# Kernel tuning notes

Hardware: AMD Instinct MI355X
Metric: run time of the kernel (lower is better)

## Reference

```python
import jax, jax.numpy as jnp
import numpy as np

C = 128
N_ATOMS = 3584          # 512 * 7 bands
DILATIONS = (1, 3, 9, 27, 81, 1)
NEG = 0.2               # leaky_relu slope used throughout the repo
B, T = 8, 2048


def lrelu(x):
    return jnp.where(x >= 0, x, NEG * x)


def setup_inputs() -> dict:
    key = jax.random.key(0)
    keys = iter(jax.random.split(key, 40))

    def rn(shape, scale=0.05):
        return jax.random.normal(next(keys), shape, jnp.float32) * scale

    # x: [B, 4, T]; channel 0 = atom index (stored as float, cast with .long() in forward),
    # channels 1:3 = (pos, amp), channel 3 = band size (unused by forward)
    atoms = jax.random.randint(next(keys), (B, 1, T), 0, N_ATOMS).astype(jnp.float32)
    pos_amp = jax.random.normal(next(keys), (B, 2, T), jnp.float32)
    band = jnp.zeros((B, 1, T), jnp.float32)
    x = jnp.concatenate([atoms, pos_amp, band], axis=1)

    nl = len(DILATIONS)
    return {
        "x": x,
        "embed_w": rn((N_ATOMS, C), 0.1),
        "posamp_w": rn((C, 2), 0.1), "posamp_b": jnp.zeros((C,), jnp.float32),
        "reduce_w": rn((C, 2 * C)), "reduce_b": jnp.zeros((C,), jnp.float32),
        "dil_w": rn((nl, C, C, 3)), "dil_b": jnp.zeros((nl, C), jnp.float32),
        "one_w": rn((nl, C, C)), "one_b": jnp.zeros((nl, C), jnp.float32),
        "atom_w1": rn((C, C)), "atom_b1": jnp.zeros((C,), jnp.float32),
        "atom_w2": rn((C, C)), "atom_b2": jnp.zeros((C,), jnp.float32),
        "atom_w3": rn((N_ATOMS, C)), "atom_b3": jnp.zeros((N_ATOMS,), jnp.float32),
        "pa_w1": rn((C, C)), "pa_b1": jnp.zeros((C,), jnp.float32),
        "pa_w2": rn((C, C)), "pa_b2": jnp.zeros((C,), jnp.float32),
        "pa_w3": rn((2, C)), "pa_b3": jnp.zeros((2,), jnp.float32),
    }


def _linear_stack(h, w1, b1, w2, b2, w3, b3):
    # LinearOutputStack(channels, 3, out_channels=...): two hidden linears with
    # leaky_relu, final linear with no activation.
    h = lrelu(h @ w1.T + b1)
    h = lrelu(h @ w2.T + b2)
    return h @ w3.T + b3


def reference(x, embed_w, posamp_w, posamp_b, reduce_w, reduce_b,
              dil_w, dil_b, one_w, one_b,
              atom_w1, atom_b1, atom_w2, atom_b2, atom_w3, atom_b3,
              pa_w1, pa_b1, pa_w2, pa_b2, pa_w3, pa_b3):
    xt = jnp.transpose(x, (0, 2, 1))                              # [B,T,4]
    idx = jax.lax.stop_gradient(xt[:, :, 0]).astype(jnp.int32)    # atom ids
    at = embed_w[idx]                                             # [B,T,C] gather
    pa = xt[:, :, 1:3] @ posamp_w.T + posamp_b                    # [B,T,C]
    h = jnp.concatenate([at, pa], axis=-1)                        # [B,T,2C]
    h = h @ reduce_w.T + reduce_b                                 # 1x1 conv == linear
    h = jnp.transpose(h, (0, 2, 1))                               # [B,C,T]

    # DilatedStack: residual blocks (dilated k=3 conv -> 1x1 conv -> +res -> lrelu)
    for i, d in enumerate(DILATIONS):
        orig = h
        y = jax.lax.conv_general_dilated(
            h, dil_w[i], window_strides=(1,), padding=[(d, d)],
            rhs_dilation=(d,), dimension_numbers=('NCH', 'OIH', 'NCH'))
        y = y + dil_b[i][None, :, None]
        y = jnp.einsum('oc,bct->bot', one_w[i], y) + one_b[i][None, :, None]
        h = lrelu(y + orig)

    ht = jnp.transpose(h, (0, 2, 1))                              # [B,T,C]
    # Original applies the output stacks over all T, then slices the last step.
    a = _linear_stack(ht, atom_w1, atom_b1, atom_w2, atom_b2, atom_w3, atom_b3)[:, -1:, :]
    pa_out = _linear_stack(ht, pa_w1, pa_b1, pa_w2, pa_b2, pa_w3, pa_b3)[:, -1:, :]
    return a, pa_out
```

## Files before the change

kernel.cpp:

```cpp
#include <hip/hip_runtime.h>

#define CCH 128
#define TLEN 2048
#define NBATCH 8
#define NATOMS 3584
#define NEG 0.2f
typedef unsigned long long ull;

#define PK1(a) ((ull)(a))
#define PK2(a,b) (PK1(a)|((ull)(b)<<7))
#define PK3(a,b,c) (PK2(a,b)|((ull)(c)<<14))
#define PK4(a,b,c,d) (PK3(a,b,c)|((ull)(d)<<21))
#define PK5(a,b,c,d,e) (PK4(a,b,c,d)|((ull)(e)<<28))

__device__ const int g_l2cols[28] = {
    9,10,18,19,27,28,36,37,45,46,54,55,63,64,
    72,73,81,82,90,91,99,100,108,109,117,118,126,127};

__device__ __forceinline__ float lrelu(float v) { return v >= 0.f ? v : NEG * v; }
__device__ __forceinline__ float dot4(float4 w, float4 x) {
    return w.x * x.x + w.y * x.y + w.z * x.z + w.w * x.w;
}

__device__ __forceinline__ float red16x4(float a0, float a1, float a2, float a3, int s) {
    a0 += __shfl_xor(a0, 8); a1 += __shfl_xor(a1, 8);
    a2 += __shfl_xor(a2, 8); a3 += __shfl_xor(a3, 8);
    a0 += __shfl_xor(a0, 4); a1 += __shfl_xor(a1, 4);
    a2 += __shfl_xor(a2, 4); a3 += __shfl_xor(a3, 4);
    float u0 = (s & 2) ? a2 : a0;
    float v0 = (s & 2) ? a0 : a2;
    u0 += __shfl_xor(v0, 2);
    float u1 = (s & 2) ? a3 : a1;
    float v1 = (s & 2) ? a1 : a3;
    u1 += __shfl_xor(v1, 2);
    float w  = (s & 1) ? u1 : u0;
    float vv = (s & 1) ? u0 : u1;
    w += __shfl_xor(vv, 1);
    return w;
}

template<int NB>
__device__ __forceinline__ void conv4(
        const float (*src)[CCH], float (*dst)[CCH], float* gout,
        ull pm, ull pc, ull pp, ull pd, int a0,
        const float* __restrict__ Wd, const float* __restrict__ bd,
        const float* __restrict__ Wo, const float* __restrict__ bo,
        float (*ybuf)[CCH], int g, int s)
{
    const int ch = 4 * g + (s & 3);
    const float myBd = bd[ch];
    const float myBo = bo[ch];
    float4 W[24], V[8];
    {
        const float4* Wr = (const float4*)Wd + (size_t)(4 * g) * 96;
        #pragma unroll
        for (int r = 0; r < 4; ++r)
            #pragma unroll
            for (int j = 0; j < 3; ++j) {
                W[r * 6 + j]     = Wr[r * 96 + 3 * s + j];
                W[r * 6 + 3 + j] = Wr[r * 96 + 3 * s + 48 + j];
            }
        const float4* Or = (const float4*)Wo + (size_t)(4 * g) * 32;
        #pragma unroll
        for (int r = 0; r < 4; ++r) {
            V[r * 2]     = Or[r * 32 + s];
            V[r * 2 + 1] = Or[r * 32 + s + 16];
        }
    }
    __syncthreads();
    #pragma unroll
    for (int t = 0; t < NB; ++t) {
        const float* fm = src[(int)((pm >> (7 * t)) & 127)];
        const float* fc = src[(int)((pc >> (7 * t)) & 127)];
        const float* fp = src[(int)((pp >> (7 * t)) & 127)];
        float4 m0 = *(const float4*)(fm + 4 * s);
        float4 m1 = *(const float4*)(fm + 4 * s + 64);
        float4 c0 = *(const float4*)(fc + 4 * s);
        float4 c1 = *(const float4*)(fc + 4 * s + 64);
        float4 p0 = *(const float4*)(fp + 4 * s);
        float4 p1 = *(const float4*)(fp + 4 * s + 64);
        float acc[4];
        #pragma unroll
        for (int r = 0; r < 4; ++r) {
            float4 wA = W[r*6+0], wB = W[r*6+1], wC = W[r*6+2];
            float a = wA.x*m0.x + wA.y*c0.x + wA.z*p0.x + wA.w*m0.y
                    + wB.x*c0.y + wB.y*p0.y + wB.z*m0.z + wB.w*c0.z
                    + wC.x*p0.z + wC.y*m0.w + wC.z*c0.w + wC.w*p0.w;
            float4 wD = W[r*6+3], wE = W[r*6+4], wF = W[r*6+5];
            float b2 = wD.x*m1.x + wD.y*c1.x + wD.z*p1.x + wD.w*m1.y
                     + wE.x*c1.y + wE.y*p1.y + wE.z*m1.z + wE.w*c1.z
                     + wF.x*p1.z + wF.y*m1.w + wF.z*c1.w + wF.w*p1.w;
            acc[r] = a + b2;
        }
        float tot = red16x4(acc[0], acc[1], acc[2], acc[3], s);
        if (s < 4) ybuf[t][ch] = tot + myBd;
    }
    __syncthreads();
    #pragma unroll
    for (int t = 0; t < NB; ++t) {
        int jc = (int)((pc >> (7 * t)) & 127);
        int jd = (int)((pd >> (7 * t)) & 127);
        const float* y = ybuf[t];
        float4 y0 = *(const float4*)(y + 4 * s);
        float4 y1 = *(const float4*)(y + 4 * s + 64);
        float a0_ = dot4(V[0], y0) + dot4(V[1], y1);
        float a1_ = dot4(V[2], y0) + dot4(V[3], y1);
        float a2_ = dot4(V[4], y0) + dot4(V[5], y1);
        float a3_ = dot4(V[6], y0) + dot4(V[7], y1);
        float tot = red16x4(a0_, a1_, a2_, a3_, s);
        if (s < 4) {
            float h = lrelu(tot + myBo + src[jc][ch]);
            if (gout) gout[ch] = h;
            else      dst[jd][ch] = (a0 + jd < 128) ? h : 0.f;
        }
    }
}

__device__ __forceinline__ void mlp4(
        const float* hin, float* hout,
        const float* __restrict__ w, const float* __restrict__ bv,
        int g, int s)
{
    const int ch = 4 * g + (s & 3);
    const float myB = bv[ch];
    float4 V[8];
    const float4* r = (const float4*)w + (size_t)(4 * g) * 32;
    #pragma unroll
    for (int rr = 0; rr < 4; ++rr) {
        V[rr * 2]     = r[rr * 32 + s];
        V[rr * 2 + 1] = r[rr * 32 + s + 16];
    }
    __syncthreads();
    float4 x0 = *(const float4*)(hin + 4 * s);
    float4 x1 = *(const float4*)(hin + 4 * s + 64);
    float a0_ = dot4(V[0], x0) + dot4(V[1], x1);
    float a1_ = dot4(V[2], x0) + dot4(V[3], x1);
    float a2_ = dot4(V[4], x0) + dot4(V[5], x1);
    float a3_ = dot4(V[6], x0) + dot4(V[7], x1);
    float tot = red16x4(a0_, a1_, a2_, a3_, s);
    if (s < 4) hout[ch] = lrelu(tot + myB);
}

__global__ void __launch_bounds__(512, 2) k_cone(
        const float* __restrict__ x,
        const float* __restrict__ embed_w,
        const float* __restrict__ posamp_w,
        const float* __restrict__ posamp_b,
        const float* __restrict__ reduce_w,
        const float* __restrict__ reduce_b,
        const float* __restrict__ dil_w,
        const float* __restrict__ dil_b,
        const float* __restrict__ one_w,
        const float* __restrict__ one_b,
        float* __restrict__ l2c)
{
    const int i   = blockIdx.x;
    const int b   = blockIdx.y;
    const int own = g_l2cols[i];
    const int a0  = own - 4;
    const int tid = threadIdx.x;
    const int g   = tid >> 4;
    const int s   = tid & 15;
    const int ch  = 4 * g + (s & 3);

    __shared__ float A[9][CCH];
    __shared__ float B[8][CCH];
    __shared__ float cat[9][2 * CCH];
    __shared__ float ybuf[3][CCH];

    const float* xb = x + b * 4 * TLEN;
    for (int v = tid; v < 9 * 256; v += 512) {
        int p   = v >> 8;
        int chv = v & 255;
        int ab  = a0 + p;
        float val = 0.f;
        if (ab < 128) {
            int t = (TLEN - 128) + ab;
            if (chv < CCH) {
                int idx = (int)xb[t];
                val = embed_w[idx * CCH + chv];
            } else {
                int cc = chv - CCH;
                val = posamp_w[2 * cc] * xb[TLEN + t]
                    + posamp_w[2 * cc + 1] * xb[2 * TLEN + t] + posamp_b[cc];
            }
        }
        cat[p][chv] = val;
    }
    float4 RW[16];
    const float4* rw = (const float4*)reduce_w + (size_t)(4 * g) * 64;
    #pragma unroll
    for (int r = 0; r < 4; ++r)
        #pragma unroll
        for (int j = 0; j < 4; ++j)
            RW[r * 4 + j] = rw[r * 64 + s + 16 * j];
    const float rb = reduce_b[ch];
    __syncthreads();

    #pragma unroll 3
    for (int t = 0; t < 9; ++t) {
        const float* sc = cat[t];
        float4 x0 = *(const float4*)(sc + 4 * s);
        float4 x1 = *(const float4*)(sc + 4 * s + 64);
        float4 x2 = *(const float4*)(sc + 4 * s + 128);
        float4 x3 = *(const float4*)(sc + 4 * s + 192);
        float a0_ = dot4(RW[0], x0) + dot4(RW[1], x1) + dot4(RW[2], x2) + dot4(RW[3], x3);
        float a1_ = dot4(RW[4], x0) + dot4(RW[5], x1) + dot4(RW[6], x2) + dot4(RW[7], x3);
        float a2_ = dot4(RW[8], x0) + dot4(RW[9], x1) + dot4(RW[10], x2) + dot4(RW[11], x3);
        float a3_ = dot4(RW[12], x0) + dot4(RW[13], x1) + dot4(RW[14], x2) + dot4(RW[15], x3);
        float tot = red16x4(a0_, a1_, a2_, a3_, s);
        if (s < 4) A[t][ch] = (a0 + t < 128) ? tot + rb : 0.f;
    }

    conv4<3>(A, B, nullptr,
             PK3(0,3,6), PK3(1,4,7), PK3(2,5,8), PK3(1,4,7), a0,
             dil_w, dil_b, one_w, one_b, ybuf, g, s);
    conv4<1>(B, B, l2c + (size_t)(b * 28 + i) * CCH,
             PK1(1), PK1(4), PK1(7), PK1(4), a0,
             dil_w + (size_t)1 * CCH * CCH * 3, dil_b + CCH,
             one_w + (size_t)1 * CCH * CCH, one_b + CCH, ybuf, g, s);
}

__global__ void __launch_bounds__(512, 2) k_tail(
        const float* __restrict__ l2c,
        const float* __restrict__ dil_w,
        const float* __restrict__ dil_b,
        const float* __restrict__ one_w,
        const float* __restrict__ one_b,
        const float* __restrict__ aw1, const float* __restrict__ ab1,
        const float* __restrict__ aw2, const float* __restrict__ ab2,
        const float* __restrict__ pw1, const float* __restrict__ pb1,
        const float* __restrict__ pw2, const float* __restrict__ pb2,
        const float* __restrict__ pw3, const float* __restrict__ pb3,
        float* __restrict__ h2w,
        float* __restrict__ out)
{
    const int b   = blockIdx.x;
    const int tid = threadIdx.x;
    const int g   = tid >> 4;
    const int s   = tid & 15;

    __shared__ float E[29][CCH];
    __shared__ float D[11][CCH];
    __shared__ float B2[5][CCH];
    __shared__ float C2[3][CCH];
    __shared__ float HF[CCH];
    __shared__ float ybuf[5][CCH];
    __shared__ float h1a[CCH], h1p[CCH], h2p[CCH];

    if (tid < CCH) { E[28][tid] = 0.f; D[10][tid] = 0.f; B2[4][tid] = 0.f; C2[2][tid] = 0.f; }
    for (int v = tid; v < 28 * 32; v += 512) {
        int col = v >> 5, f4i = v & 31;
        *(float4*)&E[col][f4i * 4] =
            *(const float4*)(l2c + (size_t)(b * 28 + col) * CCH + f4i * 4);
    }

    const float* Wd3 = dil_w + (size_t)2 * CCH * CCH * 3;
    const float* bd3 = dil_b + 2 * CCH;
    const float* Wo3 = one_w + (size_t)2 * CCH * CCH;
    const float* bo3 = one_b + 2 * CCH;
    conv4<5>(E, D, nullptr,
             PK5(0,1,6,7,12), PK5(2,3,8,9,14), PK5(4,5,10,11,16),
             PK5(0,1,2,3,4), -1000, Wd3, bd3, Wo3, bo3, ybuf, g, s);
    conv4<5>(E, D, nullptr,
             PK5(13,18,19,24,25), PK5(15,20,21,26,27), PK5(17,22,23,28,28),
             PK5(5,6,7,8,9), -1000, Wd3, bd3, Wo3, bo3, ybuf, g, s);

    conv4<4>(D, B2, nullptr,
             PK4(0,1,6,7), PK4(2,3,8,9), PK4(4,5,10,10), PK4(0,1,2,3), -1000,
             dil_w + (size_t)3 * CCH * CCH * 3, dil_b + 3 * CCH,
             one_w + (size_t)3 * CCH * CCH, one_b + 3 * CCH, ybuf, g, s);
    conv4<2>(B2, C2, nullptr,
             PK2(0,1), PK2(2,3), PK2(4,4), PK2(0,1), -1000,
             dil_w + (size_t)4 * CCH * CCH * 3, dil_b + 4 * CCH,
             one_w + (size_t)4 * CCH * CCH, one_b + 4 * CCH, ybuf, g, s);
    conv4<1>(C2, C2, HF,
             PK1(0), PK1(1), PK1(2), PK1(0), -1000,
             dil_w + (size_t)5 * CCH * CCH * 3, dil_b + 5 * CCH,
             one_w + (size_t)5 * CCH * CCH, one_b + 5 * CCH, ybuf, g, s);

    mlp4(HF, h1a, aw1, ab1, g, s);
    mlp4(HF, h1p, pw1, pb1, g, s);
    mlp4(h1a, h2w + b * CCH, aw2, ab2, g, s);
    mlp4(h1p, h2p, pw2, pb2, g, s);
    __syncthreads();

    if (tid < 64) {
        int row = tid >> 5, q = tid & 31;
        float4 w4 = *(const float4*)(pw3 + row * CCH + 4 * q);
        float4 xv = *(const float4*)(h2p + 4 * q);
        float acc = dot4(w4, xv);
        acc += __shfl_xor(acc, 1);
        acc += __shfl_xor(acc, 2);
        acc += __shfl_xor(acc, 4);
        acc += __shfl_xor(acc, 8);
        acc += __shfl_xor(acc, 16);
        if (q == 0) out[NBATCH * NATOMS + b * 2 + row] = acc + pb3[row];
    }
}

__global__ void __launch_bounds__(512) k_head(
        const float* __restrict__ h2w,
        const float* __restrict__ aw3, const float* __restrict__ ab3,
        float* __restrict__ out)
{
    const int b   = blockIdx.y;
    const int row = blockIdx.x * 512 + threadIdx.x;
    __shared__ float hs[CCH];
    if (threadIdx.x < 32)
        *(float4*)&hs[threadIdx.x * 4] =
            *(const float4*)(h2w + b * CCH + threadIdx.x * 4);
    __syncthreads();

    const float4* r = (const float4*)(aw3 + (size_t)row * CCH);
    float s0 = 0.f, s1 = 0.f, s2 = 0.f, s3 = 0.f;
    #pragma unroll
    for (int k = 0; k < 32; k += 4) {
        s0 += dot4(r[k],     *(const float4*)&hs[4 * k]);
        s1 += dot4(r[k + 1], *(const float4*)&hs[4 * k + 4]);
        s2 += dot4(r[k + 2], *(const float4*)&hs[4 * k + 8]);
        s3 += dot4(r[k + 3], *(const float4*)&hs[4 * k + 12]);
    }
    out[b * NATOMS + row] = s0 + s1 + s2 + s3 + ab3[row];
}

extern "C" void kernel_launch(void* const* d_in, const int* in_sizes, int n_in,
                              void* d_out, int out_size, void* d_ws, size_t ws_size,
                              hipStream_t stream)
{
    const float* x        = (const float*)d_in[0];
    const float* embed_w  = (const float*)d_in[1];
    const float* posamp_w = (const float*)d_in[2];
    const float* posamp_b = (const float*)d_in[3];
    const float* reduce_w = (const float*)d_in[4];
    const float* reduce_b = (const float*)d_in[5];
    const float* dil_w    = (const float*)d_in[6];
    const float* dil_b    = (const float*)d_in[7];
    const float* one_w    = (const float*)d_in[8];
    const float* one_b    = (const float*)d_in[9];
    const float* aw1 = (const float*)d_in[10]; const float* ab1 = (const float*)d_in[11];
    const float* aw2 = (const float*)d_in[12]; const float* ab2 = (const float*)d_in[13];
    const float* aw3 = (const float*)d_in[14]; const float* ab3 = (const float*)d_in[15];
    const float* pw1 = (const float*)d_in[16]; const float* pb1 = (const float*)d_in[17];
    const float* pw2 = (const float*)d_in[18]; const float* pb2 = (const float*)d_in[19];
    const float* pw3 = (const float*)d_in[20]; const float* pb3 = (const float*)d_in[21];

    float* l2c = (float*)d_ws;
    float* h2w = l2c + NBATCH * 28 * CCH;

    k_cone<<<dim3(28, NBATCH), dim3(512), 0, stream>>>(
        x, embed_w, posamp_w, posamp_b, reduce_w, reduce_b,
        dil_w, dil_b, one_w, one_b, l2c);

    k_tail<<<dim3(NBATCH), dim3(512), 0, stream>>>(
        l2c, dil_w, dil_b, one_w, one_b,
        aw1, ab1, aw2, ab2, pw1, pb1, pw2, pb2, pw3, pb3,
        h2w, (float*)d_out);

    k_head<<<dim3(7, NBATCH), dim3(512), 0, stream>>>(
        h2w, aw3, ab3, (float*)d_out);
}
```

Baseline: 61.99 us.

## Split layer-3 conv into its own wide kernel and prefetch later weights into L2

```diff
diff --git a/kernel.cpp b/kernel.cpp
--- a/kernel.cpp
+++ b/kernel.cpp
@@ -20,6 +20,14 @@
 __device__ __forceinline__ float lrelu(float v) { return v >= 0.f ? v : NEG * v; }
 __device__ __forceinline__ float dot4(float4 w, float4 x) {
     return w.x * x.x + w.y * x.y + w.z * x.z + w.w * x.w;
+}
+
+__device__ __forceinline__ void warm(const float* p, int nf4, int gid, int nthr) {
+    const float4* q = (const float4*)p;
+    for (int i = gid; i < nf4; i += nthr) {
+        float4 v = q[i];
+        asm volatile("" :: "v"(v.x), "v"(v.y), "v"(v.z), "v"(v.w));
+    }
 }
 
 __device__ __forceinline__ float red16x4(float a0, float a1, float a2, float a3, int s) {
@@ -152,6 +160,9 @@
         const float* __restrict__ dil_b,
         const float* __restrict__ one_w,
         const float* __restrict__ one_b,
+        const float* __restrict__ aw1, const float* __restrict__ aw2,
+        const float* __restrict__ pw1, const float* __restrict__ pw2,
+        const float* __restrict__ aw3,
         float* __restrict__ l2c)
 {
     const int i   = blockIdx.x;
@@ -162,6 +173,18 @@
     const int g   = tid >> 4;
     const int s   = tid & 15;
     const int ch  = 4 * g + (s & 3);
+
+    {
+        const int gid  = (b * 28 + i) * 512 + tid;
+        const int nthr = 224 * 512;
+        warm(dil_w + (size_t)2 * CCH * CCH * 3, 4 * CCH * CCH * 3 / 4, gid, nthr);
+        warm(one_w + (size_t)2 * CCH * CCH,     4 * CCH * CCH / 4,     gid, nthr);
+        warm(aw1, CCH * CCH / 4, gid, nthr);
+        warm(aw2, CCH * CCH / 4, gid, nthr);
+        warm(pw1, CCH * CCH / 4, gid, nthr);
+        warm(pw2, CCH * CCH / 4, gid, nthr);
+        warm(aw3, NATOMS * CCH / 4, gid, nthr);
+    }
 
     __shared__ float A[9][CCH];
     __shared__ float B[8][CCH];
@@ -221,8 +244,43 @@
              one_w + (size_t)1 * CCH * CCH, one_b + CCH, ybuf, g, s);
 }
 
+__global__ void __launch_bounds__(512, 2) k_l3(
+        const float* __restrict__ l2c,
+        const float* __restrict__ dil_w,
+        const float* __restrict__ dil_b,
+        const float* __restrict__ one_w,
+        const float* __restrict__ one_b,
+        float* __restrict__ d3c)
+{
+    const int i   = blockIdx.x;
+    const int b   = blockIdx.y;
+    const int tid = threadIdx.x;
+    const int g   = tid >> 4;
+    const int s   = tid & 15;
+
+    __shared__ float E3[4][CCH];
+    __shared__ float ybuf[1][CCH];
+
+    const int jm = 6 * (i >> 1) + (i & 1);
+    const bool hasp = (i < 8);
+    if (tid < CCH) E3[3][tid] = 0.f;
+    if (tid < 384) {
+        int col = tid >> 7, f4i = tid & 31;
+        int src = (col == 0) ? jm : (col == 1) ? jm + 2 : (hasp ? jm + 4 : -1);
+        float4 v = make_float4(0.f, 0.f, 0.f, 0.f);
+        if (src >= 0)
+            v = *(const float4*)(l2c + (size_t)(b * 28 + src) * CCH + f4i * 4);
+        *(float4*)&E3[col][f4i * 4] = v;
+    }
+
+    conv4<1>(E3, E3, d3c + (size_t)(b * 10 + i) * CCH,
+             PK1(0), PK1(1), PK1(2), PK1(0), -1000,
+             dil_w + (size_t)2 * CCH * CCH * 3, dil_b + 2 * CCH,
+             one_w + (size_t)2 * CCH * CCH, one_b + 2 * CCH, ybuf, g, s);
+}
+
 __global__ void __launch_bounds__(512, 2) k_tail(
-        const float* __restrict__ l2c,
+        const float* __restrict__ d3c,
         const float* __restrict__ dil_w,
         const float* __restrict__ dil_b,
         const float* __restrict__ one_w,
@@ -240,31 +298,19 @@
     const int g   = tid >> 4;
     const int s   = tid & 15;
 
-    __shared__ float E[29][CCH];
     __shared__ float D[11][CCH];
     __shared__ float B2[5][CCH];
     __shared__ float C2[3][CCH];
     __shared__ float HF[CCH];
-    __shared__ float ybuf[5][CCH];
+    __shared__ float ybuf[4][CCH];
     __shared__ float h1a[CCH], h1p[CCH], h2p[CCH];
 
-    if (tid < CCH) { E[28][tid] = 0.f; D[10][tid] = 0.f; B2[4][tid] = 0.f; C2[2][tid] = 0.f; }
-    for (int v = tid; v < 28 * 32; v += 512) {
-        int col = v >> 5, f4i = v & 31;
-        *(float4*)&E[col][f4i * 4] =
-            *(const float4*)(l2c + (size_t)(b * 28 + col) * CCH + f4i * 4);
-    }
-
-    const float* Wd3 = dil_w + (size_t)2 * CCH * CCH * 3;
-    const float* bd3 = dil_b + 2 * CCH;
-    const float* Wo3 = one_w + (size_t)2 * CCH * CCH;
-    const float* bo3 = one_b + 2 * CCH;
-    conv4<5>(E, D, nullptr,
-             PK5(0,1,6,7,12), PK5(2,3,8,9,14), PK5(4,5,10,11,16),
-             PK5(0,1,2,3,4), -1000, Wd3, bd3, Wo3, bo3, ybuf, g, s);
-    conv4<5>(E, D, nullptr,
-             PK5(13,18,19,24,25), PK5(15,20,21,26,27), PK5(17,22,23,28,28),
-             PK5(5,6,7,8,9), -1000, Wd3, bd3, Wo3, bo3, ybuf, g, s);
+    if (tid < CCH) { D[10][tid] = 0.f; B2[4][tid] = 0.f; C2[2][tid] = 0.f; }
+    if (tid < 320) {
+        int col = tid >> 5, f4i = tid & 31;
+        *(float4*)&D[col][f4i * 4] =
+            *(const float4*)(d3c + (size_t)(b * 10 + col) * CCH + f4i * 4);
+    }
 
     conv4<4>(D, B2, nullptr,
              PK4(0,1,6,7), PK4(2,3,8,9), PK4(4,5,10,10), PK4(0,1,2,3), -1000,
@@ -346,14 +392,19 @@
     const float* pw3 = (const float*)d_in[20]; const float* pb3 = (const float*)d_in[21];
 
     float* l2c = (float*)d_ws;
-    float* h2w = l2c + NBATCH * 28 * CCH;
+    float* d3c = l2c + NBATCH * 28 * CCH;
+    float* h2w = d3c + NBATCH * 10 * CCH;
 
     k_cone<<<dim3(28, NBATCH), dim3(512), 0, stream>>>(
         x, embed_w, posamp_w, posamp_b, reduce_w, reduce_b,
-        dil_w, dil_b, one_w, one_b, l2c);
+        dil_w, dil_b, one_w, one_b,
+        aw1, aw2, pw1, pw2, aw3, l2c);
+
+    k_l3<<<dim3(10, NBATCH), dim3(512), 0, stream>>>(
+        l2c, dil_w, dil_b, one_w, one_b, d3c);
 
     k_tail<<<dim3(NBATCH), dim3(512), 0, stream>>>(
-        l2c, dil_w, dil_b, one_w, one_b,
+        d3c, dil_w, dil_b, one_w, one_b,
         aw1, ab1, aw2, ab2, pw1, pb1, pw2, pb2, pw3, pb3,
         h2w, (float*)d_out);
 
```

Measured after the change: 55.22 us. 1.12x faster.

## Fuse head into tail kernel, prefetch later weights into L2 during cone

Applied to the files above, without the earlier changes.

```diff
diff --git a/kernel.cpp b/kernel.cpp
--- a/kernel.cpp
+++ b/kernel.cpp
@@ -12,6 +12,9 @@
 #define PK3(a,b,c) (PK2(a,b)|((ull)(c)<<14))
 #define PK4(a,b,c,d) (PK3(a,b,c)|((ull)(d)<<21))
 #define PK5(a,b,c,d,e) (PK4(a,b,c,d)|((ull)(e)<<28))
+#define P6(v,k) ((ull)(v)<<(6*(k)))
+#define PX10(a,b,c,d,e,f,g,h,i,j) (P6(a,0)|P6(b,1)|P6(c,2)|P6(d,3)|P6(e,4)| \
+    P6(f,5)|P6(g,6)|P6(h,7)|P6(i,8)|P6(j,9))
 
 __device__ const int g_l2cols[28] = {
     9,10,18,19,27,28,36,37,45,46,54,55,63,64,
@@ -20,6 +23,14 @@
 __device__ __forceinline__ float lrelu(float v) { return v >= 0.f ? v : NEG * v; }
 __device__ __forceinline__ float dot4(float4 w, float4 x) {
     return w.x * x.x + w.y * x.y + w.z * x.z + w.w * x.w;
+}
+
+__device__ __forceinline__ void warm(const float* p, int nf4, int gid, int nthr) {
+    const float4* q = (const float4*)p;
+    for (int i = gid; i < nf4; i += nthr) {
+        float4 v = q[i];
+        asm volatile("" :: "v"(v.x), "v"(v.y), "v"(v.z), "v"(v.w));
+    }
 }
 
 __device__ __forceinline__ float red16x4(float a0, float a1, float a2, float a3, int s) {
@@ -39,7 +50,7 @@
     return w;
 }
 
-template<int NB>
+template<int NB, int SH = 7>
 __device__ __forceinline__ void conv4(
         const float (*src)[CCH], float (*dst)[CCH], float* gout,
         ull pm, ull pc, ull pp, ull pd, int a0,
@@ -47,6 +58,7 @@
         const float* __restrict__ Wo, const float* __restrict__ bo,
         float (*ybuf)[CCH], int g, int s)
 {
+    const int MSK = (1 << SH) - 1;
     const int ch = 4 * g + (s & 3);
     const float myBd = bd[ch];
     const float myBo = bo[ch];
@@ -70,9 +82,9 @@
     __syncthreads();
     #pragma unroll
     for (int t = 0; t < NB; ++t) {
-        const float* fm = src[(int)((pm >> (7 * t)) & 127)];
-        const float* fc = src[(int)((pc >> (7 * t)) & 127)];
-        const float* fp = src[(int)((pp >> (7 * t)) & 127)];
+        const float* fm = src[(int)((pm >> (SH * t)) & MSK)];
+        const float* fc = src[(int)((pc >> (SH * t)) & MSK)];
+        const float* fp = src[(int)((pp >> (SH * t)) & MSK)];
         float4 m0 = *(const float4*)(fm + 4 * s);
         float4 m1 = *(const float4*)(fm + 4 * s + 64);
         float4 c0 = *(const float4*)(fc + 4 * s);
@@ -98,8 +110,8 @@
     __syncthreads();
     #pragma unroll
     for (int t = 0; t < NB; ++t) {
-        int jc = (int)((pc >> (7 * t)) & 127);
-        int jd = (int)((pd >> (7 * t)) & 127);
+        int jc = (int)((pc >> (SH * t)) & MSK);
+        int jd = (int)((pd >> (SH * t)) & MSK);
         const float* y = ybuf[t];
         float4 y0 = *(const float4*)(y + 4 * s);
         float4 y1 = *(const float4*)(y + 4 * s + 64);
@@ -152,6 +164,9 @@
         const float* __restrict__ dil_b,
         const float* __restrict__ one_w,
         const float* __restrict__ one_b,
+        const float* __restrict__ aw1, const float* __restrict__ aw2,
+        const float* __restrict__ pw1, const float* __restrict__ pw2,
+        const float* __restrict__ aw3,
         float* __restrict__ l2c)
 {
     const int i   = blockIdx.x;
@@ -162,6 +177,18 @@
     const int g   = tid >> 4;
     const int s   = tid & 15;
     const int ch  = 4 * g + (s & 3);
+
+    {
+        const int gid  = (b * 28 + i) * 512 + tid;
+        const int nthr = 224 * 512;
+        warm(dil_w + (size_t)2 * CCH * CCH * 3, 4 * CCH * CCH * 3 / 4, gid, nthr);
+        warm(one_w + (size_t)2 * CCH * CCH,     4 * CCH * CCH / 4,     gid, nthr);
+        warm(aw1, CCH * CCH / 4, gid, nthr);
+        warm(aw2, CCH * CCH / 4, gid, nthr);
+        warm(pw1, CCH * CCH / 4, gid, nthr);
+        warm(pw2, CCH * CCH / 4, gid, nthr);
+        warm(aw3, NATOMS * CCH / 4, gid, nthr);
+    }
 
     __shared__ float A[9][CCH];
     __shared__ float B[8][CCH];
@@ -229,13 +256,14 @@
         const float* __restrict__ one_b,
         const float* __restrict__ aw1, const float* __restrict__ ab1,
         const float* __restrict__ aw2, const float* __restrict__ ab2,
+        const float* __restrict__ aw3, const float* __restrict__ ab3,
         const float* __restrict__ pw1, const float* __restrict__ pb1,
         const float* __restrict__ pw2, const float* __restrict__ pb2,
         const float* __restrict__ pw3, const float* __restrict__ pb3,
-        float* __restrict__ h2w,
         float* __restrict__ out)
 {
-    const int b   = blockIdx.x;
+    const int g2  = blockIdx.x;
+    const int b   = blockIdx.y;
     const int tid = threadIdx.x;
     const int g   = tid >> 4;
     const int s   = tid & 15;
@@ -245,8 +273,8 @@
     __shared__ float B2[5][CCH];
     __shared__ float C2[3][CCH];
     __shared__ float HF[CCH];
-    __shared__ float ybuf[5][CCH];
-    __shared__ float h1a[CCH], h1p[CCH], h2p[CCH];
+    __shared__ float ybuf[10][CCH];
+    __shared__ float h1a[CCH], h2a[CCH], h1p[CCH], h2p[CCH];
 
     if (tid < CCH) { E[28][tid] = 0.f; D[10][tid] = 0.f; B2[4][tid] = 0.f; C2[2][tid] = 0.f; }
     for (int v = tid; v < 28 * 32; v += 512) {
@@ -255,16 +283,13 @@
             *(const float4*)(l2c + (size_t)(b * 28 + col) * CCH + f4i * 4);
     }
 
-    const float* Wd3 = dil_w + (size_t)2 * CCH * CCH * 3;
-    const float* bd3 = dil_b + 2 * CCH;
-    const float* Wo3 = one_w + (size_t)2 * CCH * CCH;
-    const float* bo3 = one_b + 2 * CCH;
-    conv4<5>(E, D, nullptr,
-             PK5(0,1,6,7,12), PK5(2,3,8,9,14), PK5(4,5,10,11,16),
-             PK5(0,1,2,3,4), -1000, Wd3, bd3, Wo3, bo3, ybuf, g, s);
-    conv4<5>(E, D, nullptr,
-             PK5(13,18,19,24,25), PK5(15,20,21,26,27), PK5(17,22,23,28,28),
-             PK5(5,6,7,8,9), -1000, Wd3, bd3, Wo3, bo3, ybuf, g, s);
+    conv4<10, 6>(E, D, nullptr,
+             PX10(0,1,6,7,12,13,18,19,24,25),
+             PX10(2,3,8,9,14,15,20,21,26,27),
+             PX10(4,5,10,11,16,17,22,23,28,28),
+             PX10(0,1,2,3,4,5,6,7,8,9), -1000,
+             dil_w + (size_t)2 * CCH * CCH * 3, dil_b + 2 * CCH,
+             one_w + (size_t)2 * CCH * CCH, one_b + 2 * CCH, ybuf, g, s);
 
     conv4<4>(D, B2, nullptr,
              PK4(0,1,6,7), PK4(2,3,8,9), PK4(4,5,10,10), PK4(0,1,2,3), -1000,
@@ -281,47 +306,35 @@
 
     mlp4(HF, h1a, aw1, ab1, g, s);
     mlp4(HF, h1p, pw1, pb1, g, s);
-    mlp4(h1a, h2w + b * CCH, aw2, ab2, g, s);
+    mlp4(h1a, h2a, aw2, ab2, g, s);
     mlp4(h1p, h2p, pw2, pb2, g, s);
     __syncthreads();
 
-    if (tid < 64) {
-        int row = tid >> 5, q = tid & 31;
-        float4 w4 = *(const float4*)(pw3 + row * CCH + 4 * q);
-        float4 xv = *(const float4*)(h2p + 4 * q);
+    if (tid < 448) {
+        int row = g2 * 448 + tid;
+        const float4* r = (const float4*)(aw3 + (size_t)row * CCH);
+        float s0 = 0.f, s1 = 0.f, s2 = 0.f, s3 = 0.f;
+        #pragma unroll
+        for (int k = 0; k < 32; k += 4) {
+            s0 += dot4(r[k],     *(const float4*)&h2a[4 * k]);
+            s1 += dot4(r[k + 1], *(const float4*)&h2a[4 * k + 4]);
+            s2 += dot4(r[k + 2], *(const float4*)&h2a[4 * k + 8]);
+            s3 += dot4(r[k + 3], *(const float4*)&h2a[4 * k + 12]);
+        }
+        out[b * NATOMS + row] = s0 + s1 + s2 + s3 + ab3[row];
+    } else if (g2 == 0 && tid >= 448 && tid < 448 + 64) {
+        int q = tid - 448;
+        int row = q >> 5, qq = q & 31;
+        float4 w4 = *(const float4*)(pw3 + row * CCH + 4 * qq);
+        float4 xv = *(const float4*)(h2p + 4 * qq);
         float acc = dot4(w4, xv);
         acc += __shfl_xor(acc, 1);
         acc += __shfl_xor(acc, 2);
         acc += __shfl_xor(acc, 4);
         acc += __shfl_xor(acc, 8);
         acc += __shfl_xor(acc, 16);
-        if (q == 0) out[NBATCH * NATOMS + b * 2 + row] = acc + pb3[row];
-    }
-}
-
-__global__ void __launch_bounds__(512) k_head(
-        const float* __restrict__ h2w,
-        const float* __restrict__ aw3, const float* __restrict__ ab3,
-        float* __restrict__ out)
-{
-    const int b   = blockIdx.y;
-    const int row = blockIdx.x * 512 + threadIdx.x;
-    __shared__ float hs[CCH];
-    if (threadIdx.x < 32)
-        *(float4*)&hs[threadIdx.x * 4] =
-            *(const float4*)(h2w + b * CCH + threadIdx.x * 4);
-    __syncthreads();
-
-    const float4* r = (const float4*)(aw3 + (size_t)row * CCH);
-    float s0 = 0.f, s1 = 0.f, s2 = 0.f, s3 = 0.f;
-    #pragma unroll
-    for (int k = 0; k < 32; k += 4) {
-        s0 += dot4(r[k],     *(const float4*)&hs[4 * k]);
-        s1 += dot4(r[k + 1], *(const float4*)&hs[4 * k + 4]);
-        s2 += dot4(r[k + 2], *(const float4*)&hs[4 * k + 8]);
-        s3 += dot4(r[k + 3], *(const float4*)&hs[4 * k + 12]);
-    }
-    out[b * NATOMS + row] = s0 + s1 + s2 + s3 + ab3[row];
+        if (qq == 0) out[NBATCH * NATOMS + b * 2 + row] = acc + pb3[row];
+    }
 }
 
 extern "C" void kernel_launch(void* const* d_in, const int* in_sizes, int n_in,
@@ -346,17 +359,14 @@
     const float* pw3 = (const float*)d_in[20]; const float* pb3 = (const float*)d_in[21];
 
     float* l2c = (float*)d_ws;
-    float* h2w = l2c + NBATCH * 28 * CCH;
 
     k_cone<<<dim3(28, NBATCH), dim3(512), 0, stream>>>(
         x, embed_w, posamp_w, posamp_b, reduce_w, reduce_b,
-        dil_w, dil_b, one_w, one_b, l2c);
-
-    k_tail<<<dim3(NBATCH), dim3(512), 0, stream>>>(
+        dil_w, dil_b, one_w, one_b,
+        aw1, aw2, pw1, pw2, aw3, l2c);
+
+    k_tail<<<dim3(8, NBATCH), dim3(512), 0, stream>>>(
         l2c, dil_w, dil_b, one_w, one_b,
-        aw1, ab1, aw2, ab2, pw1, pb1, pw2, pb2, pw3, pb3,
-        h2w, (float*)d_out);
-
-    k_head<<<dim3(7, NBATCH), dim3(512), 0, stream>>>(
-        h2w, aw3, ab3, (float*)d_out);
-}
+        aw1, ab1, aw2, ab2, aw3, ab3,
+        pw1, pb1, pw2, pb2, pw3, pb3, (float*)d_out);
+}
```

Result: faster. 52.47 us (-15.4%).
